# Optimization experiments

Hardware: AMD Instinct MI355X
Metric: run time of the kernel (lower is better)

The kernel has to match this reference:

```python
import jax, jax.numpy as jnp
import numpy as np

N = 50000; E = 800000; T = 800000; G = 64
H = 128; IEMB = 128; BAS = 8; NS = 4; NR = 6; OEH = 128; OUT = 1; NB = 4; CUT = 5.0


def envelope(x):
    # exponent=5 -> p=6: 1/x + a*x^5 + b*x^6 + c*x^7 with a=-28, b=48, c=-21
    return 1.0 / x - 28.0 * x**5 + 48.0 * x**6 - 21.0 * x**7


def setup_inputs() -> dict:
    key = jax.random.key(0)
    ks = iter(jax.random.split(key, 80))
    def w(shape, s=0.1):
        return jax.random.normal(next(ks), shape, dtype=jnp.float32) * s
    inp = {}
    inp['z'] = jax.random.randint(next(ks), (N,), 0, 100, dtype=jnp.int32)
    inp['dist'] = jax.random.uniform(next(ks), (E,), jnp.float32, 0.05, 1.0)
    inp['dist_trip'] = jax.random.uniform(next(ks), (T,), jnp.float32, 0.05, 1.0)
    inp['angle'] = jax.random.uniform(next(ks), (T,), jnp.float32, -1.0, 1.0)
    inp['edge_index'] = jax.random.randint(next(ks), (2, E), 0, N, dtype=jnp.int32)
    inp['triplets'] = jax.random.randint(next(ks), (T, 3), 0, N, dtype=jnp.int32)
    inp['batch'] = jnp.sort(jax.random.randint(next(ks), (N,), 0, G, dtype=jnp.int32))
    inp['atom_table'] = w((100, H), 1.0)
    inp['rbf_freq'] = jnp.arange(1, NR + 1, dtype=jnp.float32) * jnp.float32(np.pi)
    inp['sbf_freq'] = jnp.arange(1, NR + 1, dtype=jnp.float32) * jnp.float32(np.pi)
    inp['emb_w1'] = w((NR, IEMB)); inp['emb_b1'] = w((IEMB,), 0.01)
    inp['emb_w2'] = w((IEMB, H)); inp['emb_b2'] = w((H,), 0.01)
    inp['iw_rbf1'] = w((NB, NR, BAS)); inp['iw_rbf2'] = w((NB, BAS, H))
    inp['iw_sbf1'] = w((NB, NS * NR, BAS)); inp['iw_sbf2'] = w((NB, BAS, IEMB))
    inp['iw_t1'] = w((NB, H, IEMB)); inp['iw_t2'] = w((NB, IEMB, H)); inp['ib_t2'] = w((NB, H), 0.01)
    inp['iw_up'] = w((NB, H, H)); inp['ib_up'] = w((NB, H), 0.01)
    inp['iw_down'] = w((NB, H, H)); inp['ib_down'] = w((NB, H), 0.01)
    inp['ow_rbf'] = w((NB + 1, NR, H))
    inp['ow0'] = w((NB + 1, H, OEH)); inp['ob0'] = w((NB + 1, OEH), 0.01)
    inp['ow1'] = w((NB + 1, OEH, OEH)); inp['ob1'] = w((NB + 1, OEH), 0.01)
    inp['ow2'] = w((NB + 1, OEH, OUT)); inp['ob2'] = w((NB + 1, OUT), 0.01)
    return inp


def _forward(atom_table, rbf_freq, sbf_freq, emb_w1, emb_b1, emb_w2, emb_b2,
             iw_rbf1, iw_rbf2, iw_sbf1, iw_sbf2, iw_t1, iw_t2, ib_t2,
             iw_up, ib_up, iw_down, ib_down, ow_rbf, ow0, ob0, ow1, ob1, ow2, ob2,
             dist, dist_trip, angle, z, edge_index, triplets, batch):
    row, col = edge_index[0], edge_index[1]
    j_idx = triplets[:, 1]
    # radial basis for edges: [E, NR]
    d = dist[:, None] / CUT
    rbf_e = envelope(d) * jnp.sin(rbf_freq * d)
    # spherical basis for triplets: [T, NS*NR]
    dt = dist_trip[:, None] / CUT
    rbf_t = envelope(dt) * jnp.sin(sbf_freq * dt)
    a = angle[:, None]
    sph = jnp.concatenate([jnp.ones_like(a), a, 0.5 * (3 * a**2 - 1), 0.5 * (5 * a**3 - 3 * a)], axis=-1)
    sbf_t = (rbf_t[:, None, :] * sph[:, :, None]).reshape(a.shape[0], -1)

    x = atom_table[z]  # [N, H]
    # EmbeddingBlock: edge msg from rbf only, scattered to col
    e = jax.nn.silu(rbf_e @ emb_w1 + emb_b1) @ emb_w2 + emb_b2
    x = x + jax.ops.segment_sum(e, col, num_segments=N)

    def out_block(k, x):
        rbf_emb = rbf_e @ ow_rbf[k]            # [E, H]
        h = jax.ops.segment_sum(x[row] * rbf_emb, col, num_segments=N)
        h = jax.nn.silu(h @ ow0[k] + ob0[k])
        h = jax.nn.silu(h @ ow1[k] + ob1[k])
        return h @ ow2[k] + ob2[k]             # [N, OUT]

    P = out_block(0, x)
    for b in range(NB):
        x_up = x @ iw_up[b] + ib_up[b]
        x_down = x @ iw_down[b] + ib_down[b]
        rbf_emb = jax.nn.silu(rbf_e @ iw_rbf1[b]) @ iw_rbf2[b]      # [E, H]
        x_edge = x_up[row] * rbf_emb                                  # [E, H]
        sbf_emb = jax.nn.silu(sbf_t @ iw_sbf1[b]) @ iw_sbf2[b]      # [T, H]
        t = jax.nn.silu(x_down @ iw_t1[b]) @ iw_t2[b] + ib_t2[b]     # [N, H]
        # original: for each triplet i, x_edge += t[j]*sbf_emb[i] (broadcast over all edges)
        extra = jnp.sum(t[j_idx] * sbf_emb, axis=0)                   # [H]
        x_edge = x_edge + extra
        x = x + jax.ops.segment_sum(x_edge, col, num_segments=N)
        P = P + out_block(b + 1, x)

    counts = jax.ops.segment_sum(jnp.ones((x.shape[0],), jnp.float32), batch, num_segments=G)
    pooled = jax.ops.segment_sum(P, batch, num_segments=G) / jnp.maximum(counts, 1.0)[:, None]
    return pooled  # [G, OUT]


def reference(z, dist, dist_trip, angle, edge_index, triplets, batch, atom_table, rbf_freq, sbf_freq,
              emb_w1, emb_b1, emb_w2, emb_b2, iw_rbf1, iw_rbf2, iw_sbf1, iw_sbf2, iw_t1, iw_t2, ib_t2,
              iw_up, ib_up, iw_down, ib_down, ow_rbf, ow0, ob0, ow1, ob1, ow2, ob2):
    return _forward(atom_table, rbf_freq, sbf_freq, emb_w1, emb_b1, emb_w2, emb_b2,
                    iw_rbf1, iw_rbf2, iw_sbf1, iw_sbf2, iw_t1, iw_t2, ib_t2,
                    iw_up, ib_up, iw_down, ib_down, ow_rbf, ow0, ob0, ow1, ob1, ow2, ob2,
                    dist, dist_trip, angle, z, edge_index, triplets, batch)
```

## Files before the change

kernel.cpp:

```cpp
#include <hip/hip_runtime.h>
#include <hip/hip_fp16.h>

#define N_ 50000
#define E_ 800000
#define T_ 800000
#define G_ 64
#define H_ 128

#define NBK 782
#define NSB (NBK * 8)
#define CAPS 512
#define CHUNK 4096
#define EB ((E_ + CHUNK - 1) / CHUNK)
#define TB ((T_ + CHUNK - 1) / CHUNK)

typedef __attribute__((ext_vector_type(8))) short bf16x8;
typedef __attribute__((ext_vector_type(4))) float f32x4;
typedef _Float16 f16x2 __attribute__((ext_vector_type(2)));

__device__ __forceinline__ float siluf(float v) {
    return __fdividef(v, 1.0f + __expf(-v));
}

__device__ __forceinline__ unsigned short f2bf(float f) {
    unsigned int u = __float_as_uint(f);
    u += 0x7fffu + ((u >> 16) & 1u);
    return (unsigned short)(u >> 16);
}
__device__ __forceinline__ unsigned int f2bf2(float a, float b) {
    return (unsigned int)f2bf(a) | ((unsigned int)f2bf(b) << 16);
}
__device__ __forceinline__ float bf2f(unsigned short h) {
    return __uint_as_float(((unsigned int)h) << 16);
}
__device__ __forceinline__ float2 bf2x2(unsigned int p) {
    return make_float2(__uint_as_float(p << 16), __uint_as_float(p & 0xffff0000u));
}
__device__ __forceinline__ float fdot2f(f16x2 a, f16x2 b, float c) {
    return __builtin_amdgcn_fdot2(a, b, c, false);
}

__global__ __launch_bounds__(256) void k_bucket(const int* __restrict__ ecol,
                                                const int* __restrict__ trip,
                                                int* bcntE, unsigned int* __restrict__ ebkt,
                                                int* bcntT, unsigned int* __restrict__ tbkt) {
    __shared__ int hist[NBK];
    __shared__ int bbase[NBK];
    int blk = blockIdx.x;
    bool isE = blk < EB;
    int ebase = (isE ? blk : blk - EB) * CHUNK;
    const int nElem = isE ? E_ : T_;
    int r = blk & 7;
    int* bcnt = isE ? bcntE : bcntT;
    unsigned int* bkt = isE ? ebkt : tbkt;
    int tid = threadIdx.x;

    for (int i = tid; i < NBK; i += 256) hist[i] = 0;
    __syncthreads();

    int cols[16];
    #pragma unroll
    for (int u = 0; u < 16; ++u) {
        int idx = ebase + u * 256 + tid;
        int c = -1;
        if (idx < nElem) c = isE ? ecol[idx] : trip[3 * idx + 1];
        cols[u] = c;
        if (c >= 0) atomicAdd(&hist[c >> 6], 1);
    }
    __syncthreads();

    for (int b = tid; b < NBK; b += 256) {
        int c = hist[b];
        bbase[b] = c ? atomicAdd(&bcnt[b * 8 + r], c) : 0;
        hist[b] = 0;
    }
    __syncthreads();

    #pragma unroll
    for (int u = 0; u < 16; ++u) {
        int c = cols[u];
        if (c >= 0) {
            int bk = c >> 6;
            int off = atomicAdd(&hist[bk], 1);
            int pos = bbase[bk] + off;
            if (pos < CAPS) {
                int idx = ebase + u * 256 + tid;
                bkt[(size_t)(bk * 8 + r) * CAPS + pos] =
                    ((unsigned int)idx << 6) | (unsigned int)(c & 63);
            }
        }
    }
}

__global__ __launch_bounds__(1024) void k_scanB(const int* __restrict__ bcntE, int* bktbaseE,
                                                const int* __restrict__ bcntT, int* bktbaseT) {
    const int* bcnt = (blockIdx.x == 0) ? bcntE : bcntT;
    int* bb = (blockIdx.x == 0) ? bktbaseE : bktbaseT;
    int tid = threadIdx.x, lane = tid & 63, w = tid >> 6;
    __shared__ int wsum[16];
    int v = 0;
    if (tid < NBK) {
        #pragma unroll
        for (int s = 0; s < 8; ++s) v += min(bcnt[tid * 8 + s], CAPS);
    }
    int incl = v;
    #pragma unroll
    for (int s = 1; s < 64; s <<= 1) {
        int t = __shfl_up(incl, (unsigned)s, 64);
        if (lane >= s) incl += t;
    }
    if (lane == 63) wsum[w] = incl;
    __syncthreads();
    int wexcl = 0;
    for (int j = 0; j < w; ++j) wexcl += wsum[j];
    if (tid < NBK) bb[tid] = wexcl + incl - v;
}

__global__ __launch_bounds__(256) void k_place(const int* __restrict__ bcntE, const unsigned int* __restrict__ ebkt,
                                               const int* __restrict__ erow, const float* __restrict__ dist,
                                               const int* __restrict__ bktbaseE, int* __restrict__ rowptrE,
                                               int* __restrict__ slist, float* __restrict__ distS,
                                               const int* __restrict__ bcntT, const unsigned int* __restrict__ tbkt,
                                               const float* __restrict__ dist_trip, const float* __restrict__ angle,
                                               const int* __restrict__ bktbaseT, int* __restrict__ rowptrT,
                                               float2* __restrict__ tpay) {
    int b = blockIdx.x;
    bool isE = b < NBK;
    if (!isE) b -= NBK;
    int tid = threadIdx.x;
    __shared__ int ccnt[64];
    __shared__ int cbase[64];
    __shared__ int nb[8];
    if (tid < 64) ccnt[tid] = 0;
    const int* bcnt = isE ? bcntE : bcntT;
    const unsigned int* bkt = isE ? ebkt : tbkt;
    if (tid < 8) nb[tid] = min(bcnt[b * 8 + tid], CAPS);
    __syncthreads();
    for (int s = 0; s < 8; ++s) {
        int n = nb[s];
        const unsigned int* src = bkt + (size_t)(b * 8 + s) * CAPS;
        for (int i = tid; i < n; i += 256) atomicAdd(&ccnt[src[i] & 63u], 1);
    }
    __syncthreads();
    if (tid < 64) {
        int v = ccnt[tid];
        int incl = v;
        #pragma unroll
        for (int s = 1; s < 64; s <<= 1) {
            int t = __shfl_up(incl, (unsigned)s, 64);
            if (tid >= s) incl += t;
        }
        int base = (isE ? bktbaseE : bktbaseT)[b];
        int excl = base + incl - v;
        cbase[tid] = excl;
        int col = b * 64 + tid;
        int* rp = isE ? rowptrE : rowptrT;
        if (col <= N_) rp[col] = excl;
        ccnt[tid] = 0;
    }
    __syncthreads();
    for (int s = 0; s < 8; ++s) {
        int n = nb[s];
        const unsigned int* src = bkt + (size_t)(b * 8 + s) * CAPS;
        for (int i = tid; i < n; i += 256) {
            unsigned int rec = src[i];
            int c = (int)(rec & 63u);
            int e = (int)(rec >> 6);
            int off = atomicAdd(&ccnt[c], 1);
            int pos = cbase[c] + off;
            if (isE) {
                slist[pos] = erow[e];
                distS[pos] = dist[e];
            } else {
                tpay[pos] = make_float2(dist_trip[e], angle[e]);
            }
        }
    }
}

__global__ __launch_bounds__(256) void k_wprep(const float* __restrict__ emb_w2, const float* __restrict__ iw_down,
                                               const float* __restrict__ iw_t1, const float* __restrict__ iw_t2,
                                               const float* __restrict__ iw_up, const float* __restrict__ ow0,
                                               const float* __restrict__ ow1, unsigned short* __restrict__ Wt) {
    int mat = blockIdx.x >> 3;
    int part = blockIdx.x & 7;
    const float* src;
    if (mat == 0) src = emb_w2;
    else if (mat < 5) src = iw_down + (size_t)(mat - 1) * 16384;
    else if (mat < 9) src = iw_t1 + (size_t)(mat - 5) * 16384;
    else if (mat < 13) src = iw_t2 + (size_t)(mat - 9) * 16384;
    else if (mat < 17) src = iw_up + (size_t)(mat - 13) * 16384;
    else if (mat < 22) src = ow0 + (size_t)(mat - 17) * 16384;
    else src = ow1 + (size_t)(mat - 22) * 16384;
    unsigned short* dst = Wt + (size_t)mat * 16384;
    int base = part * 2048;
    for (int i = base + threadIdx.x; i < base + 2048; i += 256) {
        int k = i >> 7, n = i & 127;
        dst[n * 128 + k] = f2bf(src[i]);
    }
}

__global__ __launch_bounds__(256) void k_geom(const float* __restrict__ distS,
                                              const float* __restrict__ freq, const float* __restrict__ iw_rbf1,
                                              float* __restrict__ rbfS, __half* __restrict__ s8all, int n) {
    __shared__ float W1s[4][48];
    int tid = threadIdx.x;
    if (tid < 192) W1s[tid / 48][tid % 48] = iw_rbf1[tid];
    __syncthreads();
    int p = blockIdx.x * 256 + tid;
    if (p >= n) return;
    float d = distS[p] * 0.2f;
    float d2 = d * d, d4 = d2 * d2, d5 = d4 * d;
    float env = __fdividef(1.0f, d) - 28.0f * d5 + 48.0f * d5 * d - 21.0f * d5 * d2;
    float rb[6];
    #pragma unroll
    for (int r = 0; r < 6; ++r) {
        rb[r] = env * __sinf(freq[r] * d);
        rbfS[(size_t)p * 6 + r] = rb[r];
    }
    #pragma unroll
    for (int b = 0; b < 4; ++b) {
        __half out[8];
        #pragma unroll
        for (int k = 0; k < 8; ++k) {
            float u = 0.f;
            #pragma unroll
            for (int r = 0; r < 6; ++r) u += rb[r] * W1s[b][r * 8 + k];
            out[k] = __float2half(siluf(u));
        }
        *(uint4*)&s8all[((size_t)b * n + p) * 8] = *(uint4*)out;
    }
}

__global__ __launch_bounds__(256) void k_basis(const float2* __restrict__ tpay,
                                               const float* __restrict__ sfreq, __half* __restrict__ basis, int n) {
    int t = blockIdx.x * 256 + threadIdx.x;
    if (t >= n) return;
    float2 da = tpay[t];
    float d = da.x * 0.2f;
    float a = da.y;
    float d2 = d * d, d4 = d2 * d2, d5 = d4 * d;
    float env = __fdividef(1.0f, d) - 28.0f * d5 + 48.0f * d5 * d - 21.0f * d5 * d2;
    float rb[6];
    #pragma unroll
    for (int r = 0; r < 6; ++r) rb[r] = env * __sinf(sfreq[r] * d);
    float sph[4];
    sph[0] = 1.0f; sph[1] = a; sph[2] = 1.5f * a * a - 0.5f; sph[3] = 2.5f * a * a * a - 1.5f * a;
    __half out[24];
    #pragma unroll
    for (int s = 0; s < 4; ++s)
        #pragma unroll
        for (int r = 0; r < 6; ++r) out[s * 6 + r] = __float2half(sph[s] * rb[r]);
    uint4* dst = (uint4*)(basis + (size_t)t * 24);
    dst[0] = ((uint4*)out)[0];
    dst[1] = ((uint4*)out)[1];
    dst[2] = ((uint4*)out)[2];
}

__global__ __launch_bounds__(256) void k_sv4(const int* __restrict__ rowptrT, const __half* __restrict__ basis,
                                             const float* __restrict__ iw_sbf1, float* __restrict__ SV4, int n) {
    int wave = threadIdx.x >> 6, lane = threadIdx.x & 63;
    int node = blockIdx.x * 8 + wave * 2 + (lane >> 5);
    int sub = lane & 31;
    int blk = sub >> 3, k = sub & 7;
    if (node >= n) return;
    const float* W1 = iw_sbf1 + blk * 192;
    f16x2 w[12];
    #pragma unroll
    for (int j = 0; j < 12; ++j) {
        f16x2 t;
        t.x = (_Float16)W1[(2 * j) * 8 + k];
        t.y = (_Float16)W1[(2 * j + 1) * 8 + k];
        w[j] = t;
    }
    float acc = 0.f;
    int p0 = rowptrT[node], p1 = rowptrT[node + 1];
    for (int p = p0; p < p1; ++p) {
        union { uint4 q[3]; f16x2 h[12]; } bs;
        const uint4* bp = (const uint4*)(basis + (size_t)p * 24);
        bs.q[0] = bp[0]; bs.q[1] = bp[1]; bs.q[2] = bp[2];
        float u = 0.f;
        #pragma unroll
        for (int j = 0; j < 12; ++j) u = fdot2f(bs.h[j], w[j], u);
        acc += siluf(u);
    }
    SV4[((size_t)blk * n + node) * 8 + k] = acc;
}

__global__ __launch_bounds__(256) void k_init_x(const float* __restrict__ atab, const int* __restrict__ z,
                                                unsigned short* __restrict__ xh, int n) {
    int t = blockIdx.x * 256 + threadIdx.x;
    if (t >= n * 16) return;
    int node = t >> 4, q = t & 15;
    const float4* a4 = (const float4*)atab;
    float4 v0 = a4[(size_t)z[node] * 32 + q * 2];
    float4 v1 = a4[(size_t)z[node] * 32 + q * 2 + 1];
    uint4 pk;
    pk.x = f2bf2(v0.x, v0.y);
    pk.y = f2bf2(v0.z, v0.w);
    pk.z = f2bf2(v1.x, v1.y);
    pk.w = f2bf2(v1.z, v1.w);
    ((uint4*)xh)[t] = pk;
}

__global__ __launch_bounds__(256) void k_embS(const int* __restrict__ rowptr, const float* __restrict__ rbfS,
                                              const float* __restrict__ w1, const float* __restrict__ b1,
                                              unsigned short* __restrict__ SSh, int n) {
    int node = blockIdx.x * 4 + (threadIdx.x >> 6);
    int lane = threadIdx.x & 63;
    if (node >= n) return;
    int c = lane * 2;
    float wc0[6], wc1[6];
    #pragma unroll
    for (int r = 0; r < 6; ++r) { wc0[r] = w1[r * 128 + c]; wc1[r] = w1[r * 128 + c + 1]; }
    float bb0 = b1[c], bb1 = b1[c + 1];
    float a0 = 0.f, a1 = 0.f;
    int p0 = rowptr[node], p1 = rowptr[node + 1];
    for (int p = p0; p < p1; ++p) {
        const float2* r2 = (const float2*)&rbfS[(size_t)p * 6];
        float2 ra = r2[0], rbx = r2[1], rc = r2[2];
        float u0 = bb0 + ra.x * wc0[0] + ra.y * wc0[1] + rbx.x * wc0[2] + rbx.y * wc0[3] + rc.x * wc0[4] + rc.y * wc0[5];
        float u1 = bb1 + ra.x * wc1[0] + ra.y * wc1[1] + rbx.x * wc1[2] + rbx.y * wc1[3] + rc.x * wc1[4] + rc.y * wc1[5];
        a0 += siluf(u0);
        a1 += siluf(u1);
    }
    *(unsigned int*)&SSh[(size_t)node * 128 + c] = f2bf2(a0, a1);
}

template <int BIAS_MODE, bool SILU, bool ACCBF, bool ABF, bool WF32, bool WBF>
__global__ __launch_bounds__(256, 4) void k_gemm_mfma(const void* __restrict__ Ap,
                                                      const unsigned short* __restrict__ Wt,
                                                      const float* __restrict__ bias, const int* __restrict__ rp,
                                                      float* __restrict__ C, unsigned short* __restrict__ Ch, int M) {
    int tid = threadIdx.x;
    int wave = tid >> 6, lane = tid & 63;
    int m15 = lane & 15, quad = lane >> 4;
    int row0 = blockIdx.x * 64 + wave * 16;
    int arow = row0 + m15;
    if (arow > M - 1) arow = M - 1;

    f32x4 acc[8];
    #pragma unroll
    for (int nt = 0; nt < 8; ++nt) acc[nt] = (f32x4){0.f, 0.f, 0.f, 0.f};

    #pragma unroll
    for (int kt = 0; kt < 4; ++kt) {
        int ks = kt * 32 + quad * 8;
        bf16x8 av;
        if constexpr (ABF) {
            av = *(const bf16x8*)((const unsigned short*)Ap + (size_t)arow * 128 + ks);
        } else {
            const float* Arow = (const float*)Ap + (size_t)arow * 128;
            float4 a0 = *(const float4*)(Arow + ks);
            float4 a1 = *(const float4*)(Arow + ks + 4);
            union { bf16x8 v; unsigned int u[4]; } af;
            af.u[0] = f2bf2(a0.x, a0.y);
            af.u[1] = f2bf2(a0.z, a0.w);
            af.u[2] = f2bf2(a1.x, a1.y);
            af.u[3] = f2bf2(a1.z, a1.w);
            av = af.v;
        }
        #pragma unroll
        for (int nt = 0; nt < 8; ++nt) {
            bf16x8 bf = *(const bf16x8*)(Wt + (size_t)(nt * 16 + m15) * 128 + ks);
            acc[nt] = __builtin_amdgcn_mfma_f32_16x16x32_bf16(av, bf, acc[nt], 0, 0, 0);
        }
    }

    #pragma unroll
    for (int nt = 0; nt < 8; ++nt) {
        int col = nt * 16 + m15;
        float bc = 0.f;
        if constexpr (BIAS_MODE != 0) bc = bias[col];
        #pragma unroll
        for (int reg = 0; reg < 4; ++reg) {
            int row = row0 + quad * 4 + reg;
            if (row < M) {
                float v = acc[nt][reg];
                if constexpr (BIAS_MODE == 1) v += bc;
                if constexpr (BIAS_MODE == 2) v += bc * (float)(rp[row + 1] - rp[row]);
                if constexpr (SILU) v = siluf(v);
                if constexpr (ACCBF) v += bf2f(Ch[(size_t)row * 128 + col]);
                if constexpr (WF32) C[(size_t)row * 128 + col] = v;
                if constexpr (WBF) Ch[(size_t)row * 128 + col] = f2bf(v);
            }
        }
    }
}

template <int PACC>
__global__ __launch_bounds__(256, 4) void k_out_mlp(const unsigned short* __restrict__ hB,
                                                    const unsigned short* __restrict__ W0t, const float* __restrict__ b0,
                                                    const unsigned short* __restrict__ W1t, const float* __restrict__ b1,
                                                    const float* __restrict__ w2col, const float* __restrict__ ob2p,
                                                    float* __restrict__ Pout, int M) {
    __shared__ unsigned short lds[4][16 * 136];
    int tid = threadIdx.x;
    int wave = tid >> 6, lane = tid & 63;
    int m15 = lane & 15, quad = lane >> 4;
    int row0 = blockIdx.x * 64 + wave * 16;
    int arow = row0 + m15;
    if (arow > M - 1) arow = M - 1;
    unsigned short* L = lds[wave];

    f32x4 acc[8];
    #pragma unroll
    for (int nt = 0; nt < 8; ++nt) acc[nt] = (f32x4){0.f, 0.f, 0.f, 0.f};
    #pragma unroll
    for (int kt = 0; kt < 4; ++kt) {
        int ks = kt * 32 + quad * 8;
        bf16x8 av = *(const bf16x8*)(hB + (size_t)arow * 128 + ks);
        #pragma unroll
        for (int nt = 0; nt < 8; ++nt) {
            bf16x8 bf = *(const bf16x8*)(W0t + (size_t)(nt * 16 + m15) * 128 + ks);
            acc[nt] = __builtin_amdgcn_mfma_f32_16x16x32_bf16(av, bf, acc[nt], 0, 0, 0);
        }
    }
    #pragma unroll
    for (int nt = 0; nt < 8; ++nt) {
        int col = nt * 16 + m15;
        float bc = b0[col];
        #pragma unroll
        for (int reg = 0; reg < 4; ++reg)
            L[(quad * 4 + reg) * 136 + col] = f2bf(siluf(acc[nt][reg] + bc));
    }
    __syncthreads();

    #pragma unroll
    for (int nt = 0; nt < 8; ++nt) acc[nt] = (f32x4){0.f, 0.f, 0.f, 0.f};
    #pragma unroll
    for (int kt = 0; kt < 4; ++kt) {
        int ks = kt * 32 + quad * 8;
        bf16x8 av = *(const bf16x8*)(L + m15 * 136 + ks);
        #pragma unroll
        for (int nt = 0; nt < 8; ++nt) {
            bf16x8 bf = *(const bf16x8*)(W1t + (size_t)(nt * 16 + m15) * 128 + ks);
            acc[nt] = __builtin_amdgcn_mfma_f32_16x16x32_bf16(av, bf, acc[nt], 0, 0, 0);
        }
    }
    float w2c[8], pp[4];
    #pragma unroll
    for (int nt = 0; nt < 8; ++nt) w2c[nt] = w2col[nt * 16 + m15];
    #pragma unroll
    for (int reg = 0; reg < 4; ++reg) pp[reg] = 0.f;
    #pragma unroll
    for (int nt = 0; nt < 8; ++nt) {
        float bc = b1[nt * 16 + m15];
        #pragma unroll
        for (int reg = 0; reg < 4; ++reg)
            pp[reg] += siluf(acc[nt][reg] + bc) * w2c[nt];
    }
    #pragma unroll
    for (int reg = 0; reg < 4; ++reg) {
        float s = pp[reg];
        s += __shfl_xor(s, 1, 64);
        s += __shfl_xor(s, 2, 64);
        s += __shfl_xor(s, 4, 64);
        s += __shfl_xor(s, 8, 64);
        if (m15 == 0) {
            int row = row0 + quad * 4 + reg;
            if (row < M) {
                float r = s + ob2p[0];
                if constexpr (PACC == 2) r += Pout[row];
                Pout[row] = r;
            }
        }
    }
}

__global__ __launch_bounds__(256, 4) void k_block_mlp(const unsigned short* __restrict__ xh,
                                                      const unsigned short* __restrict__ Wd, const float* __restrict__ bd,
                                                      const unsigned short* __restrict__ Wt1,
                                                      const unsigned short* __restrict__ Wt2, const float* __restrict__ bt2,
                                                      const unsigned short* __restrict__ Wup, const float* __restrict__ bup,
                                                      const float* __restrict__ SV, const float* __restrict__ W2,
                                                      float* __restrict__ extra,
                                                      unsigned short* __restrict__ xuph, int M) {
    __shared__ union {
        unsigned short h[4][16 * 136];
        float f[64 * 132];
    } sm;
    int tid = threadIdx.x;
    int wave = tid >> 6, lane = tid & 63;
    int m15 = lane & 15, quad = lane >> 4;
    int row0 = blockIdx.x * 64 + wave * 16;
    int arow = row0 + m15;
    if (arow > M - 1) arow = M - 1;
    unsigned short* L = sm.h[wave];

    f32x4 accD[8], accU[8];
    #pragma unroll
    for (int nt = 0; nt < 8; ++nt) { accD[nt] = (f32x4){0.f, 0.f, 0.f, 0.f}; accU[nt] = (f32x4){0.f, 0.f, 0.f, 0.f}; }
    #pragma unroll
    for (int kt = 0; kt < 4; ++kt) {
        int ks = kt * 32 + quad * 8;
        bf16x8 av = *(const bf16x8*)(xh + (size_t)arow * 128 + ks);
        #pragma unroll
        for (int nt = 0; nt < 8; ++nt) {
            bf16x8 bd_ = *(const bf16x8*)(Wd + (size_t)(nt * 16 + m15) * 128 + ks);
            accD[nt] = __builtin_amdgcn_mfma_f32_16x16x32_bf16(av, bd_, accD[nt], 0, 0, 0);
            bf16x8 bu_ = *(const bf16x8*)(Wup + (size_t)(nt * 16 + m15) * 128 + ks);
            accU[nt] = __builtin_amdgcn_mfma_f32_16x16x32_bf16(av, bu_, accU[nt], 0, 0, 0);
        }
    }
    #pragma unroll
    for (int nt = 0; nt < 8; ++nt) {
        int col = nt * 16 + m15;
        float bcu = bup[col], bcd = bd[col];
        #pragma unroll
        for (int reg = 0; reg < 4; ++reg) {
            int row = row0 + quad * 4 + reg;
            if (row < M) xuph[(size_t)row * 128 + col] = f2bf(accU[nt][reg] + bcu);
            L[(quad * 4 + reg) * 136 + col] = f2bf(accD[nt][reg] + bcd);
        }
    }
    __syncthreads();

    #pragma unroll
    for (int nt = 0; nt < 8; ++nt) accD[nt] = (f32x4){0.f, 0.f, 0.f, 0.f};
    #pragma unroll
    for (int kt = 0; kt < 4; ++kt) {
        int ks = kt * 32 + quad * 8;
        bf16x8 av = *(const bf16x8*)(L + m15 * 136 + ks);
        #pragma unroll
        for (int nt = 0; nt < 8; ++nt) {
            bf16x8 bf = *(const bf16x8*)(Wt1 + (size_t)(nt * 16 + m15) * 128 + ks);
            accD[nt] = __builtin_amdgcn_mfma_f32_16x16x32_bf16(av, bf, accD[nt], 0, 0, 0);
        }
    }
    __syncthreads();
    #pragma unroll
    for (int nt = 0; nt < 8; ++nt) {
        int col = nt * 16 + m15;
        #pragma unroll
        for (int reg = 0; reg < 4; ++reg)
            L[(quad * 4 + reg) * 136 + col] = f2bf(siluf(accD[nt][reg]));
    }
    __syncthreads();

    #pragma unroll
    for (int nt = 0; nt < 8; ++nt) accD[nt] = (f32x4){0.f, 0.f, 0.f, 0.f};
    #pragma unroll
    for (int kt = 0; kt < 4; ++kt) {
        int ks = kt * 32 + quad * 8;
        bf16x8 av = *(const bf16x8*)(L + m15 * 136 + ks);
        #pragma unroll
        for (int nt = 0; nt < 8; ++nt) {
            bf16x8 bf = *(const bf16x8*)(Wt2 + (size_t)(nt * 16 + m15) * 128 + ks);
            accD[nt] = __builtin_amdgcn_mfma_f32_16x16x32_bf16(av, bf, accD[nt], 0, 0, 0);
        }
    }
    __syncthreads();
    #pragma unroll
    for (int nt = 0; nt < 8; ++nt) {
        int col = nt * 16 + m15;
        float bc = bt2[col];
        #pragma unroll
        for (int reg = 0; reg < 4; ++reg) {
            int lr = wave * 16 + quad * 4 + reg;
            sm.f[lr * 132 + col] = accD[nt][reg] + bc;
        }
    }
    __syncthreads();

    int col = tid & 127, half = tid >> 7;
    float acc8[8];
    #pragma unroll
    for (int k = 0; k < 8; ++k) acc8[k] = 0.f;
    int rmax = M - blockIdx.x * 64;
    if (rmax > 64) rmax = 64;
    for (int rr = half; rr < rmax; rr += 2) {
        float t = sm.f[rr * 132 + col];
        const float4* sv4 = (const float4*)&SV[(size_t)(blockIdx.x * 64 + rr) * 8];
        float4 s0 = sv4[0], s1 = sv4[1];
        acc8[0] += t * s0.x; acc8[1] += t * s0.y; acc8[2] += t * s0.z; acc8[3] += t * s0.w;
        acc8[4] += t * s1.x; acc8[5] += t * s1.y; acc8[6] += t * s1.z; acc8[7] += t * s1.w;
    }
    float e = 0.f;
    #pragma unroll
    for (int k = 0; k < 8; ++k) e += acc8[k] * W2[k * 128 + col];
    __syncthreads();
    sm.f[tid] = e;
    __syncthreads();
    if (tid < 128) atomicAdd(&extra[col], sm.f[tid] + sm.f[tid + 128]);
}

__global__ __launch_bounds__(256) void k_out_gather(const int* __restrict__ rowptr, const int* __restrict__ slist,
                                                    const float* __restrict__ rbfS,
                                                    const unsigned short* __restrict__ xh,
                                                    const float* __restrict__ wrbf,
                                                    unsigned short* __restrict__ hB, int n) {
    int node = blockIdx.x * 4 + (threadIdx.x >> 6);
    int lane = threadIdx.x & 63;
    if (node >= n) return;
    int c = lane * 2;
    float wc0[6], wc1[6];
    #pragma unroll
    for (int r = 0; r < 6; ++r) { wc0[r] = wrbf[r * 128 + c]; wc1[r] = wrbf[r * 128 + c + 1]; }
    float a0 = 0.f, a1 = 0.f;
    int p0 = rowptr[node], p1 = rowptr[node + 1];
    int p = p0;
    for (; p + 4 <= p1; p += 4) {
        int s0 = slist[p], s1 = slist[p + 1], s2 = slist[p + 2], s3 = slist[p + 3];
        float2 rb[4][3];
        #pragma unroll
        for (int u = 0; u < 4; ++u) {
            const float2* r2 = (const float2*)&rbfS[(size_t)(p + u) * 6];
            rb[u][0] = r2[0]; rb[u][1] = r2[1]; rb[u][2] = r2[2];
        }
        unsigned int xv0 = *(const unsigned int*)&xh[(size_t)s0 * 128 + c];
        unsigned int xv1 = *(const unsigned int*)&xh[(size_t)s1 * 128 + c];
        unsigned int xv2 = *(const unsigned int*)&xh[(size_t)s2 * 128 + c];
        unsigned int xv3 = *(const unsigned int*)&xh[(size_t)s3 * 128 + c];
        #pragma unroll
        for (int u = 0; u < 4; ++u) {
            float e0 = rb[u][0].x * wc0[0] + rb[u][0].y * wc0[1] + rb[u][1].x * wc0[2] +
                       rb[u][1].y * wc0[3] + rb[u][2].x * wc0[4] + rb[u][2].y * wc0[5];
            float e1 = rb[u][0].x * wc1[0] + rb[u][0].y * wc1[1] + rb[u][1].x * wc1[2] +
                       rb[u][1].y * wc1[3] + rb[u][2].x * wc1[4] + rb[u][2].y * wc1[5];
            float2 xf = bf2x2((u == 0) ? xv0 : (u == 1) ? xv1 : (u == 2) ? xv2 : xv3);
            a0 += xf.x * e0;
            a1 += xf.y * e1;
        }
    }
    for (; p < p1; ++p) {
        int src = slist[p];
        const float2* r2 = (const float2*)&rbfS[(size_t)p * 6];
        float2 ra = r2[0], rbx = r2[1], rc = r2[2];
        float e0 = ra.x * wc0[0] + ra.y * wc0[1] + rbx.x * wc0[2] + rbx.y * wc0[3] + rc.x * wc0[4] + rc.y * wc0[5];
        float e1 = ra.x * wc1[0] + ra.y * wc1[1] + rbx.x * wc1[2] + rbx.y * wc1[3] + rc.x * wc1[4] + rc.y * wc1[5];
        float2 xf = bf2x2(*(const unsigned int*)&xh[(size_t)src * 128 + c]);
        a0 += xf.x * e0;
        a1 += xf.y * e1;
    }
    *(unsigned int*)&hB[(size_t)node * 128 + c] = f2bf2(a0, a1);
}

__global__ __launch_bounds__(256) void k_interact(const int* __restrict__ rowptr, const int* __restrict__ slist,
                                                  const __half* __restrict__ s8, const float* __restrict__ W2,
                                                  const float* __restrict__ extra,
                                                  const unsigned short* __restrict__ xuph,
                                                  unsigned short* __restrict__ xh, int n) {
    int node = blockIdx.x * 4 + (threadIdx.x >> 6);
    int lane = threadIdx.x & 63;
    if (node >= n) return;
    int c = lane * 2;
    f16x2 w2a[4], w2b[4];
    #pragma unroll
    for (int j = 0; j < 4; ++j) {
        f16x2 wa, wb;
        wa.x = (_Float16)W2[(2 * j) * 128 + c];
        wa.y = (_Float16)W2[(2 * j + 1) * 128 + c];
        wb.x = (_Float16)W2[(2 * j) * 128 + c + 1];
        wb.y = (_Float16)W2[(2 * j + 1) * 128 + c + 1];
        w2a[j] = wa;
        w2b[j] = wb;
    }
    int p0 = rowptr[node], p1 = rowptr[node + 1];
    float cntf = (float)(p1 - p0);
    float a0 = cntf * extra[c], a1 = cntf * extra[c + 1];
    int p = p0;
    for (; p + 4 <= p1; p += 4) {
        int s0 = slist[p], s1 = slist[p + 1], s2 = slist[p + 2], s3 = slist[p + 3];
        uint4 sv[4];
        #pragma unroll
        for (int u = 0; u < 4; ++u) sv[u] = *(const uint4*)(s8 + (size_t)(p + u) * 8);
        unsigned int xv0 = *(const unsigned int*)&xuph[(size_t)s0 * 128 + c];
        unsigned int xv1 = *(const unsigned int*)&xuph[(size_t)s1 * 128 + c];
        unsigned int xv2 = *(const unsigned int*)&xuph[(size_t)s2 * 128 + c];
        unsigned int xv3 = *(const unsigned int*)&xuph[(size_t)s3 * 128 + c];
        #pragma unroll
        for (int u = 0; u < 4; ++u) {
            union { uint4 q; f16x2 h[4]; } s;
            s.q = sv[u];
            float e0 = fdot2f(s.h[0], w2a[0], 0.f);
            e0 = fdot2f(s.h[1], w2a[1], e0);
            e0 = fdot2f(s.h[2], w2a[2], e0);
            e0 = fdot2f(s.h[3], w2a[3], e0);
            float e1 = fdot2f(s.h[0], w2b[0], 0.f);
            e1 = fdot2f(s.h[1], w2b[1], e1);
            e1 = fdot2f(s.h[2], w2b[2], e1);
            e1 = fdot2f(s.h[3], w2b[3], e1);
            float2 xf = bf2x2((u == 0) ? xv0 : (u == 1) ? xv1 : (u == 2) ? xv2 : xv3);
            a0 += xf.x * e0;
            a1 += xf.y * e1;
        }
    }
    for (; p < p1; ++p) {
        int src = slist[p];
        float2 xf = bf2x2(*(const unsigned int*)&xuph[(size_t)src * 128 + c]);
        union { uint4 q; f16x2 h[4]; } s;
        s.q = *(const uint4*)(s8 + (size_t)p * 8);
        float e0 = fdot2f(s.h[0], w2a[0], 0.f);
        e0 = fdot2f(s.h[1], w2a[1], e0);
        e0 = fdot2f(s.h[2], w2a[2], e0);
        e0 = fdot2f(s.h[3], w2a[3], e0);
        float e1 = fdot2f(s.h[0], w2b[0], 0.f);
        e1 = fdot2f(s.h[1], w2b[1], e1);
        e1 = fdot2f(s.h[2], w2b[2], e1);
        e1 = fdot2f(s.h[3], w2b[3], e1);
        a0 += xf.x * e0;
        a1 += xf.y * e1;
    }
    unsigned int cur = *(unsigned int*)&xh[(size_t)node * 128 + c];
    float2 xc = bf2x2(cur);
    *(unsigned int*)&xh[(size_t)node * 128 + c] = f2bf2(xc.x + a0, xc.y + a1);
}

__global__ __launch_bounds__(256) void k_pool(const float* __restrict__ P, const int* __restrict__ batch,
                                              float* __restrict__ pool, float* __restrict__ cnt, int n) {
    int i = blockIdx.x * 256 + threadIdx.x;
    int lane = threadIdx.x & 63;
    int b = (i < n) ? batch[i] : -1;
    float p = (i < n) ? P[i] : 0.f;
    int b0 = __shfl(b, 0, 64);
    int b63 = __shfl(b, 63, 64);
    if (b0 == b63 && b0 >= 0) {
        float s = p;
        #pragma unroll
        for (int off = 32; off > 0; off >>= 1) s += __shfl_xor(s, off, 64);
        if (lane == 0) {
            atomicAdd(&pool[b0], s);
            atomicAdd(&cnt[b0], 64.0f);
        }
    } else {
        if (i < n) {
            atomicAdd(&pool[b], p);
            atomicAdd(&cnt[b], 1.0f);
        }
    }
}

__global__ __launch_bounds__(64) void k_final(const float* __restrict__ pool, const float* __restrict__ cnt,
                                              float* __restrict__ out) {
    int g = threadIdx.x;
    if (g < G_) out[g] = __fdividef(pool[g], fmaxf(cnt[g], 1.0f));
}

extern "C" void kernel_launch(void* const* d_in, const int* in_sizes, int n_in,
                              void* d_out, int out_size, void* d_ws, size_t ws_size,
                              hipStream_t stream) {
    (void)in_sizes; (void)n_in; (void)out_size; (void)ws_size;
    const int* z = (const int*)d_in[0];
    const float* dist = (const float*)d_in[1];
    const float* dist_trip = (const float*)d_in[2];
    const float* angle = (const float*)d_in[3];
    const int* edge_index = (const int*)d_in[4];
    const int* triplets = (const int*)d_in[5];
    const int* batch = (const int*)d_in[6];
    const float* atom_table = (const float*)d_in[7];
    const float* rbf_freq = (const float*)d_in[8];
    const float* sbf_freq = (const float*)d_in[9];
    const float* emb_w1 = (const float*)d_in[10];
    const float* emb_b1 = (const float*)d_in[11];
    const float* emb_w2 = (const float*)d_in[12];
    const float* emb_b2 = (const float*)d_in[13];
    const float* iw_rbf1 = (const float*)d_in[14];
    const float* iw_rbf2 = (const float*)d_in[15];
    const float* iw_sbf1 = (const float*)d_in[16];
    const float* iw_sbf2 = (const float*)d_in[17];
    const float* iw_t1 = (const float*)d_in[18];
    const float* iw_t2 = (const float*)d_in[19];
    const float* ib_t2 = (const float*)d_in[20];
    const float* iw_up = (const float*)d_in[21];
    const float* ib_up = (const float*)d_in[22];
    const float* iw_down = (const float*)d_in[23];
    const float* ib_down = (const float*)d_in[24];
    const float* ow_rbf = (const float*)d_in[25];
    const float* ow0 = (const float*)d_in[26];
    const float* ob0 = (const float*)d_in[27];
    const float* ow1 = (const float*)d_in[28];
    const float* ob1 = (const float*)d_in[29];
    const float* ow2 = (const float*)d_in[30];
    const float* ob2 = (const float*)d_in[31];

    const int* erow = edge_index;
    const int* ecol = edge_index + E_;

    float* ws = (float*)d_ws;
    float* bufA = ws;
    float* bufB = bufA + (size_t)N_ * H_;
    float* P = bufB + (size_t)N_ * H_;
    float* rbfS = P + N_;
    float* SV4 = rbfS + (size_t)E_ * 6;
    float* extra4 = SV4 + (size_t)4 * N_ * 8;
    float* pool = extra4 + 512;
    float* cnt = pool + G_;
    int* bcntE = (int*)(cnt + G_);
    int* bcntT = bcntE + NSB;
    int* bktbaseE = bcntT + NSB;
    int* bktbaseT = bktbaseE + NBK;
    int* rowptr = bktbaseT + NBK;
    int* rowptrT = rowptr + N_ + 1;
    int* slist = rowptrT + N_ + 1;
    float* distS = (float*)(slist + E_);
    uintptr_t tp = (uintptr_t)(distS + E_);
    tp = (tp + 7) & ~(uintptr_t)7;
    float2* tpay = (float2*)tp;
    __half* s8all = (__half*)(tpay + T_);
    __half* basis = s8all + (size_t)4 * E_ * 8;
    unsigned short* xh = (unsigned short*)(basis + (size_t)T_ * 24);
    unsigned short* xuph = xh + (size_t)N_ * H_;
    unsigned short* Wt = xuph + (size_t)N_ * H_;
    unsigned short* hB = (unsigned short*)bufB;

    unsigned int* ebkt = (unsigned int*)s8all;
    unsigned int* tbkt = ebkt + (size_t)NSB * CAPS;

    const int EG = (E_ + 255) / 256;
    const int TG = (T_ + 255) / 256;
    const int NG4 = (N_ + 3) / 4;
    const int GEMMG = (N_ + 63) / 64;

    hipMemsetAsync(extra4, 0, (512 + 2 * G_ + 2 * NSB) * sizeof(float), stream);
    k_wprep<<<27 * 8, 256, 0, stream>>>(emb_w2, iw_down, iw_t1, iw_t2, iw_up, ow0, ow1, Wt);
    k_bucket<<<EB + TB, 256, 0, stream>>>(ecol, triplets, bcntE, ebkt, bcntT, tbkt);
    k_scanB<<<2, 1024, 0, stream>>>(bcntE, bktbaseE, bcntT, bktbaseT);
    k_place<<<2 * NBK, 256, 0, stream>>>(bcntE, ebkt, erow, dist, bktbaseE, rowptr, slist, distS,
                                         bcntT, tbkt, dist_trip, angle, bktbaseT, rowptrT, tpay);

    k_geom<<<EG, 256, 0, stream>>>(distS, rbf_freq, iw_rbf1, rbfS, s8all, E_);
    k_basis<<<TG, 256, 0, stream>>>(tpay, sbf_freq, basis, T_);
    k_sv4<<<(N_ + 7) / 8, 256, 0, stream>>>(rowptrT, basis, iw_sbf1, SV4, N_);
    k_init_x<<<(N_ * 16 + 255) / 256, 256, 0, stream>>>(atom_table, z, xh, N_);

    k_embS<<<NG4, 256, 0, stream>>>(rowptr, rbfS, emb_w1, emb_b1, (unsigned short*)bufA, N_);
    k_gemm_mfma<2, false, true, true, false, true><<<GEMMG, 256, 0, stream>>>(
        bufA, Wt, emb_b2, rowptr, nullptr, xh, N_);

    auto out_block = [&](int k, bool first) {
        k_out_gather<<<NG4, 256, 0, stream>>>(rowptr, slist, rbfS, xh,
                                              ow_rbf + (size_t)k * 6 * 128, hB, N_);
        if (first)
            k_out_mlp<1><<<GEMMG, 256, 0, stream>>>(hB, Wt + (size_t)(17 + k) * 16384, ob0 + k * 128,
                                                    Wt + (size_t)(22 + k) * 16384, ob1 + k * 128,
                                                    ow2 + k * 128, ob2 + k, P, N_);
        else
            k_out_mlp<2><<<GEMMG, 256, 0, stream>>>(hB, Wt + (size_t)(17 + k) * 16384, ob0 + k * 128,
                                                    Wt + (size_t)(22 + k) * 16384, ob1 + k * 128,
                                                    ow2 + k * 128, ob2 + k, P, N_);
    };

    out_block(0, true);

    for (int b = 0; b < 4; ++b) {
        k_block_mlp<<<GEMMG, 256, 0, stream>>>(xh,
                                               Wt + (size_t)(1 + b) * 16384, ib_down + b * 128,
                                               Wt + (size_t)(5 + b) * 16384,
                                               Wt + (size_t)(9 + b) * 16384, ib_t2 + b * 128,
                                               Wt + (size_t)(13 + b) * 16384, ib_up + b * 128,
                                               SV4 + (size_t)b * N_ * 8,
                                               iw_sbf2 + (size_t)b * 1024,
                                               extra4 + b * 128,
                                               xuph, N_);
        k_interact<<<NG4, 256, 0, stream>>>(rowptr, slist, s8all + (size_t)b * E_ * 8,
                                            iw_rbf2 + (size_t)b * 1024, extra4 + b * 128,
                                            xuph, xh, N_);
        out_block(b + 1, false);
    }

    k_pool<<<(N_ + 255) / 256, 256, 0, stream>>>(P, batch, pool, cnt, N_);
    k_final<<<1, 64, 0, stream>>>(pool, cnt, (float*)d_out);
}
```

Baseline: 1.508 ms.

## Halve MFMA GEMM block size and spread extra-term atomics over slots

```diff
diff --git a/kernel.cpp b/kernel.cpp
--- a/kernel.cpp
+++ b/kernel.cpp
@@ -13,6 +13,7 @@
 #define CHUNK 4096
 #define EB ((E_ + CHUNK - 1) / CHUNK)
 #define TB ((T_ + CHUNK - 1) / CHUNK)
+#define XSLOT 16
 
 typedef __attribute__((ext_vector_type(8))) short bf16x8;
 typedef __attribute__((ext_vector_type(4))) float f32x4;
@@ -328,14 +329,14 @@
 }
 
 template <int BIAS_MODE, bool SILU, bool ACCBF, bool ABF, bool WF32, bool WBF>
-__global__ __launch_bounds__(256, 4) void k_gemm_mfma(const void* __restrict__ Ap,
-                                                      const unsigned short* __restrict__ Wt,
-                                                      const float* __restrict__ bias, const int* __restrict__ rp,
-                                                      float* __restrict__ C, unsigned short* __restrict__ Ch, int M) {
+__global__ __launch_bounds__(128) void k_gemm_mfma(const void* __restrict__ Ap,
+                                                   const unsigned short* __restrict__ Wt,
+                                                   const float* __restrict__ bias, const int* __restrict__ rp,
+                                                   float* __restrict__ C, unsigned short* __restrict__ Ch, int M) {
     int tid = threadIdx.x;
     int wave = tid >> 6, lane = tid & 63;
     int m15 = lane & 15, quad = lane >> 4;
-    int row0 = blockIdx.x * 64 + wave * 16;
+    int row0 = blockIdx.x * 32 + wave * 16;
     int arow = row0 + m15;
     if (arow > M - 1) arow = M - 1;
 
@@ -389,16 +390,16 @@
 }
 
 template <int PACC>
-__global__ __launch_bounds__(256, 4) void k_out_mlp(const unsigned short* __restrict__ hB,
-                                                    const unsigned short* __restrict__ W0t, const float* __restrict__ b0,
-                                                    const unsigned short* __restrict__ W1t, const float* __restrict__ b1,
-                                                    const float* __restrict__ w2col, const float* __restrict__ ob2p,
-                                                    float* __restrict__ Pout, int M) {
-    __shared__ unsigned short lds[4][16 * 136];
+__global__ __launch_bounds__(128) void k_out_mlp(const unsigned short* __restrict__ hB,
+                                                 const unsigned short* __restrict__ W0t, const float* __restrict__ b0,
+                                                 const unsigned short* __restrict__ W1t, const float* __restrict__ b1,
+                                                 const float* __restrict__ w2col, const float* __restrict__ ob2p,
+                                                 float* __restrict__ Pout, int M) {
+    __shared__ unsigned short lds[2][16 * 136];
     int tid = threadIdx.x;
     int wave = tid >> 6, lane = tid & 63;
     int m15 = lane & 15, quad = lane >> 4;
-    int row0 = blockIdx.x * 64 + wave * 16;
+    int row0 = blockIdx.x * 32 + wave * 16;
     int arow = row0 + m15;
     if (arow > M - 1) arow = M - 1;
     unsigned short* L = lds[wave];
@@ -468,22 +469,22 @@
     }
 }
 
-__global__ __launch_bounds__(256, 4) void k_block_mlp(const unsigned short* __restrict__ xh,
-                                                      const unsigned short* __restrict__ Wd, const float* __restrict__ bd,
-                                                      const unsigned short* __restrict__ Wt1,
-                                                      const unsigned short* __restrict__ Wt2, const float* __restrict__ bt2,
-                                                      const unsigned short* __restrict__ Wup, const float* __restrict__ bup,
-                                                      const float* __restrict__ SV, const float* __restrict__ W2,
-                                                      float* __restrict__ extra,
-                                                      unsigned short* __restrict__ xuph, int M) {
+__global__ __launch_bounds__(128) void k_block_mlp(const unsigned short* __restrict__ xh,
+                                                   const unsigned short* __restrict__ Wd, const float* __restrict__ bd,
+                                                   const unsigned short* __restrict__ Wt1,
+                                                   const unsigned short* __restrict__ Wt2, const float* __restrict__ bt2,
+                                                   const unsigned short* __restrict__ Wup, const float* __restrict__ bup,
+                                                   const float* __restrict__ SV, const float* __restrict__ W2,
+                                                   float* __restrict__ extraP,
+                                                   unsigned short* __restrict__ xuph, int M) {
     __shared__ union {
-        unsigned short h[4][16 * 136];
-        float f[64 * 132];
+        unsigned short h[2][16 * 136];
+        float f[32 * 132];
     } sm;
     int tid = threadIdx.x;
     int wave = tid >> 6, lane = tid & 63;
     int m15 = lane & 15, quad = lane >> 4;
-    int row0 = blockIdx.x * 64 + wave * 16;
+    int row0 = blockIdx.x * 32 + wave * 16;
     int arow = row0 + m15;
     if (arow > M - 1) arow = M - 1;
     unsigned short* L = sm.h[wave];
@@ -563,15 +564,15 @@
     }
     __syncthreads();
 
-    int col = tid & 127, half = tid >> 7;
+    int col = tid;
     float acc8[8];
     #pragma unroll
     for (int k = 0; k < 8; ++k) acc8[k] = 0.f;
-    int rmax = M - blockIdx.x * 64;
-    if (rmax > 64) rmax = 64;
-    for (int rr = half; rr < rmax; rr += 2) {
+    int rmax = M - blockIdx.x * 32;
+    if (rmax > 32) rmax = 32;
+    for (int rr = 0; rr < rmax; ++rr) {
         float t = sm.f[rr * 132 + col];
-        const float4* sv4 = (const float4*)&SV[(size_t)(blockIdx.x * 64 + rr) * 8];
+        const float4* sv4 = (const float4*)&SV[(size_t)(blockIdx.x * 32 + rr) * 8];
         float4 s0 = sv4[0], s1 = sv4[1];
         acc8[0] += t * s0.x; acc8[1] += t * s0.y; acc8[2] += t * s0.z; acc8[3] += t * s0.w;
         acc8[4] += t * s1.x; acc8[5] += t * s1.y; acc8[6] += t * s1.z; acc8[7] += t * s1.w;
@@ -579,10 +580,7 @@
     float e = 0.f;
     #pragma unroll
     for (int k = 0; k < 8; ++k) e += acc8[k] * W2[k * 128 + col];
-    __syncthreads();
-    sm.f[tid] = e;
-    __syncthreads();
-    if (tid < 128) atomicAdd(&extra[col], sm.f[tid] + sm.f[tid + 128]);
+    atomicAdd(&extraP[(blockIdx.x & (XSLOT - 1)) * 128 + col], e);
 }
 
 __global__ __launch_bounds__(256) void k_out_gather(const int* __restrict__ rowptr, const int* __restrict__ slist,
@@ -638,11 +636,20 @@
 
 __global__ __launch_bounds__(256) void k_interact(const int* __restrict__ rowptr, const int* __restrict__ slist,
                                                   const __half* __restrict__ s8, const float* __restrict__ W2,
-                                                  const float* __restrict__ extra,
+                                                  const float* __restrict__ extraP,
                                                   const unsigned short* __restrict__ xuph,
                                                   unsigned short* __restrict__ xh, int n) {
-    int node = blockIdx.x * 4 + (threadIdx.x >> 6);
-    int lane = threadIdx.x & 63;
+    __shared__ float exs[128];
+    int tid = threadIdx.x;
+    if (tid < 128) {
+        float s = 0.f;
+        #pragma unroll
+        for (int q = 0; q < XSLOT; ++q) s += extraP[q * 128 + tid];
+        exs[tid] = s;
+    }
+    __syncthreads();
+    int node = blockIdx.x * 4 + (tid >> 6);
+    int lane = tid & 63;
     if (node >= n) return;
     int c = lane * 2;
     f16x2 w2a[4], w2b[4];
@@ -658,7 +665,7 @@
     }
     int p0 = rowptr[node], p1 = rowptr[node + 1];
     float cntf = (float)(p1 - p0);
-    float a0 = cntf * extra[c], a1 = cntf * extra[c + 1];
+    float a0 = cntf * exs[c], a1 = cntf * exs[c + 1];
     int p = p0;
     for (; p + 4 <= p1; p += 4) {
         int s0 = slist[p], s1 = slist[p + 1], s2 = slist[p + 2], s3 = slist[p + 3];
@@ -784,7 +791,7 @@
     float* rbfS = P + N_;
     float* SV4 = rbfS + (size_t)E_ * 6;
     float* extra4 = SV4 + (size_t)4 * N_ * 8;
-    float* pool = extra4 + 512;
+    float* pool = extra4 + 4 * XSLOT * 128;
     float* cnt = pool + G_;
     int* bcntE = (int*)(cnt + G_);
     int* bcntT = bcntE + NSB;
@@ -810,9 +817,9 @@
     const int EG = (E_ + 255) / 256;
     const int TG = (T_ + 255) / 256;
     const int NG4 = (N_ + 3) / 4;
-    const int GEMMG = (N_ + 63) / 64;
-
-    hipMemsetAsync(extra4, 0, (512 + 2 * G_ + 2 * NSB) * sizeof(float), stream);
+    const int GEMMG2 = (N_ + 31) / 32;
+
+    hipMemsetAsync(extra4, 0, (4 * XSLOT * 128 + 2 * G_ + 2 * NSB) * sizeof(float), stream);
     k_wprep<<<27 * 8, 256, 0, stream>>>(emb_w2, iw_down, iw_t1, iw_t2, iw_up, ow0, ow1, Wt);
     k_bucket<<<EB + TB, 256, 0, stream>>>(ecol, triplets, bcntE, ebkt, bcntT, tbkt);
     k_scanB<<<2, 1024, 0, stream>>>(bcntE, bktbaseE, bcntT, bktbaseT);
@@ -825,36 +832,36 @@
     k_init_x<<<(N_ * 16 + 255) / 256, 256, 0, stream>>>(atom_table, z, xh, N_);
 
     k_embS<<<NG4, 256, 0, stream>>>(rowptr, rbfS, emb_w1, emb_b1, (unsigned short*)bufA, N_);
-    k_gemm_mfma<2, false, true, true, false, true><<<GEMMG, 256, 0, stream>>>(
+    k_gemm_mfma<2, false, true, true, false, true><<<GEMMG2, 128, 0, stream>>>(
         bufA, Wt, emb_b2, rowptr, nullptr, xh, N_);
 
     auto out_block = [&](int k, bool first) {
         k_out_gather<<<NG4, 256, 0, stream>>>(rowptr, slist, rbfS, xh,
                                               ow_rbf + (size_t)k * 6 * 128, hB, N_);
         if (first)
-            k_out_mlp<1><<<GEMMG, 256, 0, stream>>>(hB, Wt + (size_t)(17 + k) * 16384, ob0 + k * 128,
-                                                    Wt + (size_t)(22 + k) * 16384, ob1 + k * 128,
-                                                    ow2 + k * 128, ob2 + k, P, N_);
+            k_out_mlp<1><<<GEMMG2, 128, 0, stream>>>(hB, Wt + (size_t)(17 + k) * 16384, ob0 + k * 128,
+                                                     Wt + (size_t)(22 + k) * 16384, ob1 + k * 128,
+                                                     ow2 + k * 128, ob2 + k, P, N_);
         else
-            k_out_mlp<2><<<GEMMG, 256, 0, stream>>>(hB, Wt + (size_t)(17 + k) * 16384, ob0 + k * 128,
-                                                    Wt + (size_t)(22 + k) * 16384, ob1 + k * 128,
-                                                    ow2 + k * 128, ob2 + k, P, N_);
+            k_out_mlp<2><<<GEMMG2, 128, 0, stream>>>(hB, Wt + (size_t)(17 + k) * 16384, ob0 + k * 128,
+                                                     Wt + (size_t)(22 + k) * 16384, ob1 + k * 128,
+                                                     ow2 + k * 128, ob2 + k, P, N_);
     };
 
     out_block(0, true);
 
     for (int b = 0; b < 4; ++b) {
-        k_block_mlp<<<GEMMG, 256, 0, stream>>>(xh,
-                                               Wt + (size_t)(1 + b) * 16384, ib_down + b * 128,
-                                               Wt + (size_t)(5 + b) * 16384,
-                                               Wt + (size_t)(9 + b) * 16384, ib_t2 + b * 128,
-                                               Wt + (size_t)(13 + b) * 16384, ib_up + b * 128,
-                                               SV4 + (size_t)b * N_ * 8,
-                                               iw_sbf2 + (size_t)b * 1024,
-                                               extra4 + b * 128,
-                                               xuph, N_);
+        k_block_mlp<<<GEMMG2, 128, 0, stream>>>(xh,
+                                                Wt + (size_t)(1 + b) * 16384, ib_down + b * 128,
+                                                Wt + (size_t)(5 + b) * 16384,
+                                                Wt + (size_t)(9 + b) * 16384, ib_t2 + b * 128,
+                                                Wt + (size_t)(13 + b) * 16384, ib_up + b * 128,
+                                                SV4 + (size_t)b * N_ * 8,
+                                                iw_sbf2 + (size_t)b * 1024,
+                                                extra4 + (size_t)b * XSLOT * 128,
+                                                xuph, N_);
         k_interact<<<NG4, 256, 0, stream>>>(rowptr, slist, s8all + (size_t)b * E_ * 8,
-                                            iw_rbf2 + (size_t)b * 1024, extra4 + b * 128,
+                                            iw_rbf2 + (size_t)b * 1024, extra4 + (size_t)b * XSLOT * 128,
                                             xuph, xh, N_);
         out_block(b + 1, false);
     }
```

New measurement: 1.441 ms. 1.05x faster.
